# Kernel optimization log

Hardware: AMD Instinct MI355X
Metric: run time of the kernel (lower is better)

Reference implementation:

```python
import jax, jax.numpy as jnp
import numpy as np

B = 32          # batch size
M = 32          # manifold_dim = phase_dim // 2
H = 128         # hidden_dim
EPS = 1e-6


def _init(k, shape, fan_in):
    return jax.random.normal(k, shape, jnp.float32) / np.sqrt(fan_in)


def setup_inputs() -> dict:
    key = jax.random.key(0)
    ks = jax.random.split(key, 12)
    return {
        "points": jax.random.normal(ks[0], (B, M), jnp.float32),
        # metric_network: M -> H -> M*M (ReLU)
        "Wm1": _init(ks[1], (M, H), M), "bm1": jnp.zeros((H,), jnp.float32),
        "Wm2": _init(ks[2], (H, M * M), H), "bm2": jnp.zeros((M * M,), jnp.float32),
        # christoffel_network: 3 -> H -> 1 (Tanh)
        "Wc1": _init(ks[3], (3, H), 3), "bc1": jnp.zeros((H,), jnp.float32),
        "Wc2": _init(ks[4], (H, 1), H), "bc2": jnp.zeros((1,), jnp.float32),
        # ricci_network: 4M -> 2H -> M*M (ReLU)
        "Wr1": _init(ks[5], (4 * M, 2 * H), 4 * M), "br1": jnp.zeros((2 * H,), jnp.float32),
        "Wr2": _init(ks[6], (2 * H, M * M), 2 * H), "br2": jnp.zeros((M * M,), jnp.float32),
        # flow_network: 2M -> H -> M (ReLU)
        "Wf1": _init(ks[7], (2 * M, H), 2 * M), "bf1": jnp.zeros((H,), jnp.float32),
        "Wf2": _init(ks[8], (H, M), H), "bf2": jnp.zeros((M,), jnp.float32),
        # hamiltonian MLP: 2M -> H -> 2M (Tanh)
        "Wh1": _init(ks[9], (2 * M, H), 2 * M), "bh1": jnp.zeros((H,), jnp.float32),
        "Wh2": _init(ks[10], (H, 2 * M), H), "bh2": jnp.zeros((2 * M,), jnp.float32),
    }


def _geometric_flow(points, Wm1, bm1, Wm2, bm2, Wc1, bc1, Wc2, bc2,
                    Wr1, br1, Wr2, br2, Wf1, bf1, Wf2, bf2, Wh1, bh1, Wh2, bh2):
    b = points.shape[0]
    # --- metric: (b, M, M), symmetrized, eps-regularized ---
    comps = jax.nn.relu(points @ Wm1 + bm1) @ Wm2 + bm2
    metric = comps.reshape(b, M, M) + EPS * jnp.eye(M, dtype=points.dtype)
    metric = 0.5 * (metric + jnp.swapaxes(metric, -1, -2))

    # --- Christoffel: batch over all (i,j,k) triples in one GEMM pass ---
    g_ij = jnp.broadcast_to(metric[:, :, :, None], (b, M, M, M))               # g[i,j]
    g_jk = jnp.broadcast_to(metric[:, None, :, :], (b, M, M, M))               # g[j,k]
    g_ki = jnp.broadcast_to(jnp.swapaxes(metric, 1, 2)[:, :, None, :], (b, M, M, M))  # g[k,i]
    c_in = jnp.stack([g_ij, g_jk, g_ki], axis=-1)                               # (b,M,M,M,3)
    chris = (jnp.tanh(c_in @ Wc1 + bc1) @ Wc2 + bc2)[..., 0]                    # (b,M,M,M)

    # --- Ricci: batch over all (i,j) pairs ---
    pts_b = jnp.broadcast_to(points[:, None, None, :], (b, M, M, M))
    gi = jnp.broadcast_to(metric[:, :, None, :], (b, M, M, M))   # metric[:, i]
    gj = jnp.broadcast_to(metric[:, None, :, :], (b, M, M, M))   # metric[:, j]
    r_in = jnp.concatenate([pts_b, gi, gj, chris], axis=-1)       # (b,M,M,4M)
    r_out = (jax.nn.relu(r_in @ Wr1 + br1) @ Wr2 + br2).reshape(b, M, M, M, M)
    r_out = 0.5 * (r_out + jnp.swapaxes(r_out, -1, -2))
    ricci = r_out.sum(axis=(1, 2)) / (M * M)                      # (b,M,M)

    # --- flow vector ---
    ricci_dir = jnp.einsum('bij,bj->bi', ricci, points)
    f_in = jnp.concatenate([points, ricci_dir], axis=-1)
    flow_vec = jax.nn.relu(f_in @ Wf1 + bf1) @ Wf2 + bf2

    new_pos = points + flow_vec
    phase = jnp.concatenate([new_pos, jnp.zeros_like(points)], axis=-1)  # (b, 2M)

    # --- Hamiltonian evolution (MLP stand-in) ---
    evolved = jnp.tanh(phase @ Wh1 + bh1) @ Wh2 + bh2
    return evolved


def reference(points, Wm1, bm1, Wm2, bm2, Wc1, bc1, Wc2, bc2,
              Wr1, br1, Wr2, br2, Wf1, bf1, Wf2, bf2, Wh1, bh1, Wh2, bh2):
    return _geometric_flow(points, Wm1, bm1, Wm2, bm2, Wc1, bc1, Wc2, bc2,
                           Wr1, br1, Wr2, br2, Wf1, bf1, Wf2, bf2, Wh1, bh1, Wh2, bh2)
```

## Files before the change

kernel.cpp:

```cpp
#include <hip/hip_runtime.h>

#define B 32
#define M 32
#define H 128
#define EPS 1e-6f
#define TSCALE 2.8853900817779268f

typedef float v2f __attribute__((ext_vector_type(2)));
typedef float v4f __attribute__((ext_vector_type(4)));

static __device__ __forceinline__ v2f splat2(float x) { return (v2f){x, x}; }
static __device__ __forceinline__ v4f splat4(float x) { return (v4f){x, x, x, x}; }
static __device__ __forceinline__ v2f fma2(v2f a, v2f b, v2f c) {
    return __builtin_elementwise_fma(a, b, c);
}
static __device__ __forceinline__ v4f fma4(v4f a, v4f b, v4f c) {
    return __builtin_elementwise_fma(a, b, c);
}


#define FMA4(P, s, W) \
    P.x = fmaf((s), (W).x, P.x); P.y = fmaf((s), (W).y, P.y); \
    P.z = fmaf((s), (W).z, P.z); P.w = fmaf((s), (W).w, P.w);

__global__ __launch_bounds__(256) void k_prep(
    const float* __restrict__ points, const float* __restrict__ Wm1,
    const float* __restrict__ bm1, const float* __restrict__ Wm2,
    const float* __restrict__ bm2, const float* __restrict__ Wr1,
    const float* __restrict__ br1, const float* __restrict__ bc1,
    const float* __restrict__ Wc2, const float* __restrict__ bc2,
    const float* __restrict__ Wr2, const float* __restrict__ br2,
    float* __restrict__ metric, float* __restrict__ mj,
    float* __restrict__ S, float* __restrict__ bc1s, float* __restrict__ Kc,
    int* __restrict__ cnt, float* __restrict__ Wp, float* __restrict__ c2,
    float* __restrict__ bmi_pre)
{
    __shared__ float sbuf[3392];
    const int role = blockIdx.x, t = threadIdx.x;

    if (role >= B) {
        const int u = role - B;
        float* row    = sbuf;
        float* rowsym = sbuf + 1056;
        float* ps     = sbuf + 2208;
        const float* src = (u < 256) ? (Wr2 + u * 1024) : br2;
        #pragma unroll
        for (int r = 0; r < 4; ++r) {
            const int d = t + 256 * r;
            row[(d >> 5) * 33 + (d & 31)] = src[d];
            ps[(d >> 5) * 36 + (d & 31)]  = points[d];
        }
        __syncthreads();
        #pragma unroll
        for (int r = 0; r < 4; ++r) {
            const int d = t + 256 * r, ii = d >> 5, jj = d & 31;
            rowsym[ii * 36 + jj] = 0.5f * (row[ii * 33 + jj] + row[jj * 33 + ii]);
        }
        __syncthreads();
        const int b = t >> 3, i0 = (t & 7) * 4;
        const float4* rs4 = (const float4*)rowsym;
        const float4* p4  = (const float4*)(ps + b * 36);
        float4 o; o.x = o.y = o.z = o.w = 0.f;
        #pragma unroll
        for (int m = 0; m < 8; ++m) {
            const float4 pv = p4[m];
            const float4 r0 = rs4[(i0 + 0) * 9 + m];
            const float4 r1 = rs4[(i0 + 1) * 9 + m];
            const float4 r2 = rs4[(i0 + 2) * 9 + m];
            const float4 r3 = rs4[(i0 + 3) * 9 + m];
            o.x = fmaf(pv.x, r0.x, fmaf(pv.y, r0.y, fmaf(pv.z, r0.z, fmaf(pv.w, r0.w, o.x))));
            o.y = fmaf(pv.x, r1.x, fmaf(pv.y, r1.y, fmaf(pv.z, r1.z, fmaf(pv.w, r1.w, o.y))));
            o.z = fmaf(pv.x, r2.x, fmaf(pv.y, r2.y, fmaf(pv.z, r2.z, fmaf(pv.w, r2.w, o.z))));
            o.w = fmaf(pv.x, r3.x, fmaf(pv.y, r3.y, fmaf(pv.z, r3.z, fmaf(pv.w, r3.w, o.w))));
        }
        if (u < 256) ((float4*)(Wp + u * 1024 + b * 32))[t & 7] = o;
        else         ((float4*)(c2 + b * 32))[t & 7] = o;
        return;
    }

    const int b = role;
    float* p     = sbuf;
    float* h     = sbuf + 32;
    float* comps = sbuf + 160;
    float* msym  = sbuf + 1216;
    if (t < M) p[t] = points[b * M + t];
    __syncthreads();
    if (t < H) {
        float acc = bm1[t];
        #pragma unroll
        for (int m = 0; m < M; ++m) acc = fmaf(p[m], Wm1[m * H + t], acc);
        h[t] = fmaxf(acc, 0.f);
    }
    __syncthreads();
    {
        float4 acc = ((const float4*)bm2)[t];
        const float4* Wm2_4 = (const float4*)Wm2;
        const float4* h4 = (const float4*)h;
        #pragma unroll 2
        for (int u4 = 0; u4 < 32; ++u4) {
            const float4 hv = h4[u4];
            const float4 w0 = Wm2_4[(u4 * 4 + 0) * 256 + t];
            const float4 w1 = Wm2_4[(u4 * 4 + 1) * 256 + t];
            const float4 w2 = Wm2_4[(u4 * 4 + 2) * 256 + t];
            const float4 w3 = Wm2_4[(u4 * 4 + 3) * 256 + t];
            FMA4(acc, hv.x, w0); FMA4(acc, hv.y, w1);
            FMA4(acc, hv.z, w2); FMA4(acc, hv.w, w3);
        }
        const int row = t >> 3, col0 = (t & 7) * 4;
        comps[row * 33 + col0 + 0] = acc.x;
        comps[row * 33 + col0 + 1] = acc.y;
        comps[row * 33 + col0 + 2] = acc.z;
        comps[row * 33 + col0 + 3] = acc.w;
    }
    __syncthreads();
    {
        const int row = t >> 3, col0 = (t & 7) * 4;
        #pragma unroll
        for (int c = 0; c < 4; ++c) {
            const int d = 4 * t + c, ii = row, jj = col0 + c;
            float v = 0.5f * (comps[ii * 33 + jj] + comps[jj * 33 + ii]) + (ii == jj ? EPS : 0.f);
            metric[b * M * M + d] = v;
            msym[d] = v;
        }
    }
    S[b * 256 + t] = 0.f;
    if (t == 0) cnt[b] = 0;
    __syncthreads();
    float wreg[M], wreg2[M];
    #pragma unroll
    for (int m = 0; m < M; ++m) {
        wreg[m]  = Wr1[(64 + m) * 256 + t];
        wreg2[m] = Wr1[(32 + m) * 256 + t];
    }
    float pbr = br1[t];
    #pragma unroll
    for (int m = 0; m < M; ++m) pbr = fmaf(p[m], Wr1[m * 256 + t], pbr);
    const float4* msym4 = (const float4*)msym;
    for (int x = 0; x < M; ++x) {
        float acc = 0.f, acc2 = pbr;
        #pragma unroll
        for (int mq = 0; mq < 8; ++mq) {
            float4 mv = msym4[x * 8 + mq];
            acc  = fmaf(mv.x, wreg[4 * mq + 0], acc);
            acc  = fmaf(mv.y, wreg[4 * mq + 1], acc);
            acc  = fmaf(mv.z, wreg[4 * mq + 2], acc);
            acc  = fmaf(mv.w, wreg[4 * mq + 3], acc);
            acc2 = fmaf(mv.x, wreg2[4 * mq + 0], acc2);
            acc2 = fmaf(mv.y, wreg2[4 * mq + 1], acc2);
            acc2 = fmaf(mv.z, wreg2[4 * mq + 2], acc2);
            acc2 = fmaf(mv.w, wreg2[4 * mq + 3], acc2);
        }
        mj[(b * M + x) * 256 + t] = acc;
        bmi_pre[(b * M + x) * 256 + t] = acc2;
    }
    if (b == 0) {
        if (t < H) bc1s[t] = bc1[t] * TSCALE;
        if (t == 0) {
            float s = bc2[0];
            for (int u = 0; u < H; ++u) s += Wc2[u];
            Kc[0] = s;
        }
    }
}

__global__ __launch_bounds__(512) void k_main(
    const float* __restrict__ points, const float* __restrict__ metric,
    const float* __restrict__ mj, const float* __restrict__ bmi_pre,
    const float* __restrict__ Wc1, const float* __restrict__ Wc2,
    const float* __restrict__ bc1s, const float* __restrict__ Kc,
    const float* __restrict__ Wr1, float* __restrict__ S,
    int* __restrict__ cnt,
    const float* __restrict__ Wp, const float* __restrict__ c2,
    const float* __restrict__ Wf1, const float* __restrict__ bf1,
    const float* __restrict__ Wf2, const float* __restrict__ bf2,
    const float* __restrict__ Wh1, const float* __restrict__ bh1,
    const float* __restrict__ Wh2, const float* __restrict__ bh2,
    float* __restrict__ out)
{
    const int blk = blockIdx.x;
    const int b = blk & 31, i = blk >> 5;
    const int t = threadIdx.x;
    const int w = t >> 6, l = t & 63;
    const int ph = l >> 5, k = l & 31;

    __shared__ float chlds[8 * 128];
    __shared__ float Slds[256];
    __shared__ int finflag;

    const float* mb = metric + b * 1024;
    const int j0 = 2 * w + ph, j1 = 16 + 2 * w + ph;
    const float gki  = mb[i * M + k] * TSCALE;
    const v2f gijv = {mb[i * M + j0] * TSCALE, mb[i * M + j1] * TSCALE};
    const v2f gjkv = {mb[j0 * M + k] * TSCALE, mb[j1 * M + k] * TSCALE};
    const v4f* mj4 = (const v4f*)(mj + b * M * 256);
    const int jb = w * 2;
    v4f p00 = mj4[(jb + 0) * 64 + l];
    v4f p01 = mj4[(jb + 1) * 64 + l];
    v4f p10 = mj4[(jb + 16) * 64 + l];
    v4f p11 = mj4[(jb + 17) * 64 + l];
    const v4f bmiv = ((const v4f*)(bmi_pre + (b * M + i) * 256))[l];
    if (t < 256) Slds[t] = 0.f;

    v2f acc2 = {0.f, 0.f};
    #pragma unroll 8
    for (int u = 0; u < H; ++u) {
        const float tc = fmaf(gki, Wc1[2 * H + u], bc1s[u]);
        v2f pre = fma2(gijv, splat2(Wc1[u]), fma2(gjkv, splat2(Wc1[H + u]), splat2(tc)));
        v2f e = {__builtin_amdgcn_exp2f(pre.x), __builtin_amdgcn_exp2f(pre.y)};
        e += (v2f){1.f, 1.f};
        const v2f r = {__builtin_amdgcn_rcpf(e.x), __builtin_amdgcn_rcpf(e.y)};
        acc2 = fma2(r, splat2(Wc2[u]), acc2);
    }
    const float KcV = Kc[0];
    chlds[w * 128 + k * 4 + ph]     = fmaf(-2.f, acc2.x, KcV);
    chlds[w * 128 + k * 4 + 2 + ph] = fmaf(-2.f, acc2.y, KcV);

    const v4f* wg = (const v4f*)(Wr1 + 96 * 256);
    const v4f* ch4 = (const v4f*)(chlds + w * 128);
    p00 += bmiv; p01 += bmiv; p10 += bmiv; p11 += bmiv;

    #define STEP(W, kk) { \
        const v4f s = ch4[kk]; \
        p00 = fma4(splat4(s.x), W, p00); p01 = fma4(splat4(s.y), W, p01); \
        p10 = fma4(splat4(s.z), W, p10); p11 = fma4(splat4(s.w), W, p11); }

    #pragma unroll
    for (int kc = 0; kc < 8; ++kc) {
        const int kb = kc * 4;
        const v4f w0 = wg[(kb + 0) * 64 + l];
        const v4f w1 = wg[(kb + 1) * 64 + l];
        const v4f w2 = wg[(kb + 2) * 64 + l];
        const v4f w3 = wg[(kb + 3) * 64 + l];
        STEP(w0, kb + 0) STEP(w1, kb + 1) STEP(w2, kb + 2) STEP(w3, kb + 3)
    }
    #undef STEP

    const v4f z4 = {0.f, 0.f, 0.f, 0.f};
    const v4f r00 = __builtin_elementwise_max(p00, z4);
    const v4f r01 = __builtin_elementwise_max(p01, z4);
    const v4f r10 = __builtin_elementwise_max(p10, z4);
    const v4f r11 = __builtin_elementwise_max(p11, z4);
    const v4f rs = (r00 + r01) + (r10 + r11);
    atomicAdd(&Slds[4*l + 0], rs.x);
    atomicAdd(&Slds[4*l + 1], rs.y);
    atomicAdd(&Slds[4*l + 2], rs.z);
    atomicAdd(&Slds[4*l + 3], rs.w);
    __syncthreads();
    if (t < 256) atomicAdd(&S[b * 256 + t], Slds[t]);
    asm volatile("s_waitcnt vmcnt(0)" ::: "memory");
    __syncthreads();
    if (t == 0) {
        int old = atomicAdd(&cnt[b], 1);
        finflag = (old == 31);
    }
    __syncthreads();
    if (!finflag) return;

    float* fs   = chlds;
    float* rdp  = chlds + 256;
    float* pl   = chlds + 768;
    float* fin  = chlds + 800;
    float* hf   = chlds + 864;
    float* npos = Slds;
    float* hh   = Slds + 32;

    if (t < 256) fs[t] = atomicAdd(&S[b * 256 + t], 0.f) * (1.f / 1024.f);
    if (t < M) pl[t] = points[b * M + t];
    __syncthreads();
    {
        const int ii = t & 31, ch = t >> 5;
        float part = 0.f;
        #pragma unroll
        for (int uu = 0; uu < 16; ++uu) {
            const int u = ch * 16 + uu;
            part = fmaf(fs[u], Wp[u * 1024 + b * 32 + ii], part);
        }
        rdp[t] = part;
    }
    __syncthreads();
    if (t < M) {
        float a = c2[b * 32 + t];
        #pragma unroll
        for (int ch = 0; ch < 16; ++ch) a += rdp[ch * 32 + t];
        fin[t] = pl[t];
        fin[M + t] = a;
    }
    __syncthreads();
    if (t < H) {
        float acc = bf1[t];
        #pragma unroll
        for (int m = 0; m < 2 * M; ++m) acc = fmaf(fin[m], Wf1[m * H + t], acc);
        hf[t] = fmaxf(acc, 0.f);
    }
    __syncthreads();
    if (t < M) {
        float acc = bf2[t];
        #pragma unroll
        for (int u = 0; u < H; ++u) acc = fmaf(hf[u], Wf2[u * M + t], acc);
        npos[t] = pl[t] + acc;
    }
    __syncthreads();
    if (t < H) {
        float acc = bh1[t];
        #pragma unroll
        for (int m = 0; m < M; ++m) acc = fmaf(npos[m], Wh1[m * H + t], acc);
        hh[t] = tanhf(acc);
    }
    __syncthreads();
    if (t < 2 * M) {
        float acc = bh2[t];
        #pragma unroll
        for (int u = 0; u < H; ++u) acc = fmaf(hh[u], Wh2[u * (2 * M) + t], acc);
        out[b * (2 * M) + t] = acc;
    }
}

extern "C" void kernel_launch(void* const* d_in, const int* in_sizes, int n_in,
                              void* d_out, int out_size, void* d_ws, size_t ws_size,
                              hipStream_t stream)
{
    const float* points = (const float*)d_in[0];
    const float* Wm1 = (const float*)d_in[1];
    const float* bm1 = (const float*)d_in[2];
    const float* Wm2 = (const float*)d_in[3];
    const float* bm2 = (const float*)d_in[4];
    const float* Wc1 = (const float*)d_in[5];
    const float* bc1 = (const float*)d_in[6];
    const float* Wc2 = (const float*)d_in[7];
    const float* bc2 = (const float*)d_in[8];
    const float* Wr1 = (const float*)d_in[9];
    const float* br1 = (const float*)d_in[10];
    const float* Wr2 = (const float*)d_in[11];
    const float* br2 = (const float*)d_in[12];
    const float* Wf1 = (const float*)d_in[13];
    const float* bf1 = (const float*)d_in[14];
    const float* Wf2 = (const float*)d_in[15];
    const float* bf2 = (const float*)d_in[16];
    const float* Wh1 = (const float*)d_in[17];
    const float* bh1 = (const float*)d_in[18];
    const float* Wh2 = (const float*)d_in[19];
    const float* bh2 = (const float*)d_in[20];
    float* out = (float*)d_out;

    float* ws      = (float*)d_ws;
    float* metric  = ws;
    float* mj      = ws + 32768;
    float* S       = ws + 294912;
    float* bc1s    = ws + 303104;
    float* Kc      = ws + 303232;
    int*   cnt     = (int*)(ws + 303236);
    float* Wp      = ws + 303268;
    float* c2      = ws + 565412;
    float* bmi_pre = ws + 566436;

    k_prep<<<289, 256, 0, stream>>>(points, Wm1, bm1, Wm2, bm2, Wr1, br1, bc1,
                                    Wc2, bc2, Wr2, br2, metric, mj, S, bc1s,
                                    Kc, cnt, Wp, c2, bmi_pre);
    k_main<<<B * M, 512, 0, stream>>>(points, metric, mj, bmi_pre, Wc1, Wc2,
                                      bc1s, Kc, Wr1, S, cnt,
                                      Wp, c2, Wf1, bf1, Wf2, bf2,
                                      Wh1, bh1, Wh2, bh2, out);
}
```

Baseline: 57.76 us.

## Process two i rows per block in k_main to reuse weight and mj loads

Each k_main block now handles two consecutive i indices instead of one, which halves the grid to B*16 blocks and adjusts the completion counter threshold to match. Loads of Wc1/Wc2 scalars, the gjk term, the mj rows and the Wr1 tiles are shared across both i values, so global and LDS traffic per unit of work drops. The cost is more live registers (eight v4f accumulators), a doubled LDS buffer, and fewer blocks on the GPU, which may lower occupancy and parallelism.

Measured after the change: 59.11 us. 2.3% more time.

```diff
diff --git a/kernel.cpp b/kernel.cpp
--- a/kernel.cpp
+++ b/kernel.cpp
@@ -178,51 +178,69 @@
     float* __restrict__ out)
 {
     const int blk = blockIdx.x;
-    const int b = blk & 31, i = blk >> 5;
+    const int b = blk & 31, g = blk >> 5;
+    const int i0 = 2 * g, i1 = 2 * g + 1;
     const int t = threadIdx.x;
     const int w = t >> 6, l = t & 63;
     const int ph = l >> 5, k = l & 31;
 
-    __shared__ float chlds[8 * 128];
+    __shared__ float chlds[8 * 256];
     __shared__ float Slds[256];
     __shared__ int finflag;
 
     const float* mb = metric + b * 1024;
     const int j0 = 2 * w + ph, j1 = 16 + 2 * w + ph;
-    const float gki  = mb[i * M + k] * TSCALE;
-    const v2f gijv = {mb[i * M + j0] * TSCALE, mb[i * M + j1] * TSCALE};
-    const v2f gjkv = {mb[j0 * M + k] * TSCALE, mb[j1 * M + k] * TSCALE};
+    const float gki0 = mb[i0 * M + k] * TSCALE;
+    const float gki1 = mb[i1 * M + k] * TSCALE;
+    const v2f gij0v = {mb[i0 * M + j0] * TSCALE, mb[i0 * M + j1] * TSCALE};
+    const v2f gij1v = {mb[i1 * M + j0] * TSCALE, mb[i1 * M + j1] * TSCALE};
+    const v2f gjkv  = {mb[j0 * M + k] * TSCALE, mb[j1 * M + k] * TSCALE};
     const v4f* mj4 = (const v4f*)(mj + b * M * 256);
     const int jb = w * 2;
-    v4f p00 = mj4[(jb + 0) * 64 + l];
-    v4f p01 = mj4[(jb + 1) * 64 + l];
-    v4f p10 = mj4[(jb + 16) * 64 + l];
-    v4f p11 = mj4[(jb + 17) * 64 + l];
-    const v4f bmiv = ((const v4f*)(bmi_pre + (b * M + i) * 256))[l];
+    const v4f m0 = mj4[(jb + 0) * 64 + l];
+    const v4f m1 = mj4[(jb + 1) * 64 + l];
+    const v4f m2 = mj4[(jb + 16) * 64 + l];
+    const v4f m3 = mj4[(jb + 17) * 64 + l];
+    const v4f bmiv0 = ((const v4f*)(bmi_pre + (b * M + i0) * 256))[l];
+    const v4f bmiv1 = ((const v4f*)(bmi_pre + (b * M + i1) * 256))[l];
     if (t < 256) Slds[t] = 0.f;
 
-    v2f acc2 = {0.f, 0.f};
-    #pragma unroll 8
+    v2f accA = {0.f, 0.f}, accB = {0.f, 0.f};
+    #pragma unroll 4
     for (int u = 0; u < H; ++u) {
-        const float tc = fmaf(gki, Wc1[2 * H + u], bc1s[u]);
-        v2f pre = fma2(gijv, splat2(Wc1[u]), fma2(gjkv, splat2(Wc1[H + u]), splat2(tc)));
-        v2f e = {__builtin_amdgcn_exp2f(pre.x), __builtin_amdgcn_exp2f(pre.y)};
-        e += (v2f){1.f, 1.f};
-        const v2f r = {__builtin_amdgcn_rcpf(e.x), __builtin_amdgcn_rcpf(e.y)};
-        acc2 = fma2(r, splat2(Wc2[u]), acc2);
+        const float w1u = Wc1[u], w2u = Wc1[H + u], w3u = Wc1[2 * H + u];
+        const float c2u = Wc2[u];
+        const v2f base = fma2(gjkv, splat2(w2u), splat2(bc1s[u]));
+        v2f pre0 = fma2(gij0v, splat2(w1u), fma2(splat2(gki0), splat2(w3u), base));
+        v2f pre1 = fma2(gij1v, splat2(w1u), fma2(splat2(gki1), splat2(w3u), base));
+        v2f e0 = {__builtin_amdgcn_exp2f(pre0.x), __builtin_amdgcn_exp2f(pre0.y)};
+        v2f e1 = {__builtin_amdgcn_exp2f(pre1.x), __builtin_amdgcn_exp2f(pre1.y)};
+        e0 += (v2f){1.f, 1.f};
+        e1 += (v2f){1.f, 1.f};
+        const v2f r0 = {__builtin_amdgcn_rcpf(e0.x), __builtin_amdgcn_rcpf(e0.y)};
+        const v2f r1 = {__builtin_amdgcn_rcpf(e1.x), __builtin_amdgcn_rcpf(e1.y)};
+        accA = fma2(r0, splat2(c2u), accA);
+        accB = fma2(r1, splat2(c2u), accB);
     }
     const float KcV = Kc[0];
-    chlds[w * 128 + k * 4 + ph]     = fmaf(-2.f, acc2.x, KcV);
-    chlds[w * 128 + k * 4 + 2 + ph] = fmaf(-2.f, acc2.y, KcV);
+    float* chw = chlds + w * 256;
+    chw[k * 4 + ph]           = fmaf(-2.f, accA.x, KcV);
+    chw[k * 4 + 2 + ph]       = fmaf(-2.f, accA.y, KcV);
+    chw[128 + k * 4 + ph]     = fmaf(-2.f, accB.x, KcV);
+    chw[128 + k * 4 + 2 + ph] = fmaf(-2.f, accB.y, KcV);
 
     const v4f* wg = (const v4f*)(Wr1 + 96 * 256);
-    const v4f* ch4 = (const v4f*)(chlds + w * 128);
-    p00 += bmiv; p01 += bmiv; p10 += bmiv; p11 += bmiv;
+    const v4f* chA = (const v4f*)chw;
+    const v4f* chB = chA + 32;
+    v4f a0 = m0 + bmiv0, a1 = m1 + bmiv0, a2 = m2 + bmiv0, a3 = m3 + bmiv0;
+    v4f b0 = m0 + bmiv1, b1 = m1 + bmiv1, b2 = m2 + bmiv1, b3 = m3 + bmiv1;
 
     #define STEP(W, kk) { \
-        const v4f s = ch4[kk]; \
-        p00 = fma4(splat4(s.x), W, p00); p01 = fma4(splat4(s.y), W, p01); \
-        p10 = fma4(splat4(s.z), W, p10); p11 = fma4(splat4(s.w), W, p11); }
+        const v4f sA = chA[kk]; const v4f sB = chB[kk]; \
+        a0 = fma4(splat4(sA.x), W, a0); a1 = fma4(splat4(sA.y), W, a1); \
+        a2 = fma4(splat4(sA.z), W, a2); a3 = fma4(splat4(sA.w), W, a3); \
+        b0 = fma4(splat4(sB.x), W, b0); b1 = fma4(splat4(sB.y), W, b1); \
+        b2 = fma4(splat4(sB.z), W, b2); b3 = fma4(splat4(sB.w), W, b3); }
 
     #pragma unroll
     for (int kc = 0; kc < 8; ++kc) {
@@ -236,11 +254,10 @@
     #undef STEP
 
     const v4f z4 = {0.f, 0.f, 0.f, 0.f};
-    const v4f r00 = __builtin_elementwise_max(p00, z4);
-    const v4f r01 = __builtin_elementwise_max(p01, z4);
-    const v4f r10 = __builtin_elementwise_max(p10, z4);
-    const v4f r11 = __builtin_elementwise_max(p11, z4);
-    const v4f rs = (r00 + r01) + (r10 + r11);
+    v4f rs = __builtin_elementwise_max(a0, z4) + __builtin_elementwise_max(a1, z4)
+           + __builtin_elementwise_max(a2, z4) + __builtin_elementwise_max(a3, z4)
+           + __builtin_elementwise_max(b0, z4) + __builtin_elementwise_max(b1, z4)
+           + __builtin_elementwise_max(b2, z4) + __builtin_elementwise_max(b3, z4);
     atomicAdd(&Slds[4*l + 0], rs.x);
     atomicAdd(&Slds[4*l + 1], rs.y);
     atomicAdd(&Slds[4*l + 2], rs.z);
@@ -251,7 +268,7 @@
     __syncthreads();
     if (t == 0) {
         int old = atomicAdd(&cnt[b], 1);
-        finflag = (old == 31);
+        finflag = (old == 15);
     }
     __syncthreads();
     if (!finflag) return;
@@ -356,8 +373,8 @@
     k_prep<<<289, 256, 0, stream>>>(points, Wm1, bm1, Wm2, bm2, Wr1, br1, bc1,
                                     Wc2, bc2, Wr2, br2, metric, mj, S, bc1s,
                                     Kc, cnt, Wp, c2, bmi_pre);
-    k_main<<<B * M, 512, 0, stream>>>(points, metric, mj, bmi_pre, Wc1, Wc2,
-                                      bc1s, Kc, Wr1, S, cnt,
-                                      Wp, c2, Wf1, bf1, Wf2, bf2,
-                                      Wh1, bh1, Wh2, bh2, out);
-}
+    k_main<<<B * 16, 512, 0, stream>>>(points, metric, mj, bmi_pre, Wc1, Wc2,
+                                       bc1s, Kc, Wr1, S, cnt,
+                                       Wp, c2, Wf1, bf1, Wf2, bf2,
+                                       Wh1, bh1, Wh2, bh2, out);
+}
```
